# Kernel tuning notes

Hardware: AMD Instinct MI355X
Metric: run time of the kernel (lower is better)

The kernel has to match this reference:

```python
import jax, jax.numpy as jnp
import numpy as np

NUM_AGENTS = 1000
N_ACTIONS = 16
HIDDEN = 256
COMM_STEPS = 4
B, M = 1024, 64


def setup_inputs() -> dict:
    key = jax.random.key(0)
    ks = jax.random.split(key, 8)
    agent_ids = jax.random.randint(ks[0], (B, M), 0, NUM_AGENTS)
    emb = jax.random.normal(ks[1], (NUM_AGENTS, HIDDEN), dtype=jnp.float32) * 0.1
    s1 = 1.0 / np.sqrt(3 * HIDDEN)
    W1 = jax.random.uniform(ks[2], (3 * HIDDEN, HIDDEN), jnp.float32, -s1, s1)
    b1 = jax.random.uniform(ks[3], (HIDDEN,), jnp.float32, -s1, s1)
    s2 = 1.0 / np.sqrt(HIDDEN)
    W2 = jax.random.uniform(ks[4], (HIDDEN, HIDDEN), jnp.float32, -s2, s2)
    b2 = jax.random.uniform(ks[5], (HIDDEN,), jnp.float32, -s2, s2)
    Wd = jax.random.uniform(ks[6], (HIDDEN, N_ACTIONS), jnp.float32, -s2, s2)
    bd = jax.random.uniform(ks[7], (N_ACTIONS,), jnp.float32, -s2, s2)
    return {"agent_ids": agent_ids, "emb": emb, "W1": W1, "b1": b1,
            "W2": W2, "b2": b2, "Wd": Wd, "bd": bd}


def reference(agent_ids, emb, W1, b1, W2, b2, Wd, bd):
    # h0: (B, M, H) embedding lookup
    h0 = emb[agent_ids]
    h = h0
    m = agent_ids.shape[1]
    inv = 1.0 / (m - 1)
    for _ in range(COMM_STEPS):
        # mean of other agents' hidden states: c_j = (sum_k h_k - h_j)/(M-1)
        c = (jnp.sum(h, axis=1, keepdims=True) - h) * inv
        x = jnp.concatenate([h, c, h0], axis=-1)  # (B, M, 3H)
        delta = jax.nn.relu(jnp.einsum('bmi,ih->bmh', x, W1) + b1)
        delta = jnp.einsum('bmi,ih->bmh', delta, W2) + b2
        h = h + delta  # residual (use_skip=True)
    logits = jnp.einsum('bmh,ha->bma', h, Wd) + bd
    return logits
```

## Files before the change

kernel.cpp:

```cpp
#include <hip/hip_runtime.h>

#define HID 256
#define NB 1024
#define NACT 16

typedef __bf16 bf16x8 __attribute__((ext_vector_type(8)));
typedef float  f32x4  __attribute__((ext_vector_type(4)));

#define HA_LO   32768
#define OV      65536
#define LDS_TOT 72704

#define PREP_N (4 * 65536 + 4096)

__device__ __forceinline__ unsigned short f2bf(float x) {
    union { __bf16 b; unsigned short u; } v; v.b = (__bf16)x; return v.u;
}
__device__ __forceinline__ float bf2f(unsigned short u) {
    union { unsigned short u; __bf16 b; } v; v.u = u; return (float)v.b;
}
__device__ __forceinline__ float b2f_lo(unsigned v) { return bf2f((unsigned short)(v & 0xffffu)); }
__device__ __forceinline__ float b2f_hi(unsigned v) { return bf2f((unsigned short)(v >> 16)); }
__device__ __forceinline__ unsigned pack2(float a, float b) {
    return (unsigned)f2bf(a) | ((unsigned)f2bf(b) << 16);
}

__global__ __launch_bounds__(256) void prep_k(const float* __restrict__ W1,
                                              const float* __restrict__ W2,
                                              const float* __restrict__ Wd,
                                              unsigned short* __restrict__ WAh, unsigned short* __restrict__ WAl,
                                              unsigned short* __restrict__ WHh, unsigned short* __restrict__ WHl,
                                              unsigned short* __restrict__ WBh, unsigned short* __restrict__ WBl,
                                              unsigned short* __restrict__ WDh, unsigned short* __restrict__ WDl,
                                              float* __restrict__ Wc) {
    int i = blockIdx.x * 256 + threadIdx.x;
    const float inv = 1.0f / 63.0f;
    if (i < 3 * 65536) {
        int mat = i >> 16, j = i & 65535;
        int kq = j >> 13, r = j & 8191;
        int nb = r >> 9, r2 = r & 511;
        int l = r2 >> 3, e = r2 & 7;
        int n = nb * 16 + (l & 15);
        int k = kq * 32 + (l >> 4) * 8 + e;
        float val;
        if (mat == 0)      val = W1[k * 256 + n] - inv * W1[(256 + k) * 256 + n];
        else if (mat == 1) val = W1[(512 + k) * 256 + n];
        else               val = W2[k * 256 + n];
        unsigned short hi = f2bf(val);
        unsigned short lo = f2bf(val - bf2f(hi));
        if (mat == 0)      { WAh[j] = hi; WAl[j] = lo; }
        else if (mat == 1) { WHh[j] = hi; WHl[j] = lo; }
        else               { WBh[j] = hi; WBl[j] = lo; }
    } else if (i < 4 * 65536) {
        int j = i - 3 * 65536, k = j >> 8, n = j & 255;
        Wc[j] = inv * W1[(256 + k) * 256 + n];
    } else if (i < PREP_N) {
        int j = i - 4 * 65536, a = j >> 8, k = j & 255;
        float val = Wd[k * 16 + a];
        unsigned short hi = f2bf(val);
        WDh[j] = hi; WDl[j] = f2bf(val - bf2f(hi));
    }
}

__device__ __forceinline__ void kloopL2(const unsigned short* __restrict__ Wfh,
                                        const unsigned short* __restrict__ Wfl,
                                        const char* hA, f32x4 (&acc)[4][2],
                                        int w, int lane, int l15, int g)
{
    const int rxA = (l15 & 7) << 4;
    const size_t lbase = ((size_t)(w * 2) * 64 + lane) * 8;
    #pragma unroll 2
    for (int kq = 0; kq < 8; ++kq) {
        const int cb = (kq * 64 + g * 16) ^ rxA;
        bf16x8 ah[4], al[4];
        #pragma unroll
        for (int mt = 0; mt < 4; ++mt) {
            int rb = (mt * 16 + l15) * 512;
            ah[mt] = *(const bf16x8*)(hA + rb + cb);
            al[mt] = *(const bf16x8*)(hA + HA_LO + rb + cb);
        }
        const size_t kb = (size_t)kq * 8192 + lbase;
        #pragma unroll
        for (int nt = 0; nt < 2; ++nt) {
            bf16x8 bh = *(const bf16x8*)(Wfh + kb + nt * 512);
            bf16x8 bl = *(const bf16x8*)(Wfl + kb + nt * 512);
            #pragma unroll
            for (int mt = 0; mt < 4; ++mt) {
                acc[mt][nt] = __builtin_amdgcn_mfma_f32_16x16x32_bf16(bh, ah[mt], acc[mt][nt], 0, 0, 0);
                acc[mt][nt] = __builtin_amdgcn_mfma_f32_16x16x32_bf16(bh, al[mt], acc[mt][nt], 0, 0, 0);
                acc[mt][nt] = __builtin_amdgcn_mfma_f32_16x16x32_bf16(bl, ah[mt], acc[mt][nt], 0, 0, 0);
            }
        }
    }
}

__device__ __forceinline__ void STfun(char* lds, const float* __restrict__ Wc, int tid)
{
    char* hA = lds;
    float* Sp = (float*)(lds + OV);
    float* Sf = (float*)(lds + OV + 4096);
    float* Tp = (float*)(lds + OV + 5120);
    __syncthreads();
    {
        int ww = tid & 127, gq = tid >> 7;
        float s0 = 0.f, s1 = 0.f;
        #pragma unroll 4
        for (int m = gq * 16; m < gq * 16 + 16; ++m) {
            int byte = m * 512 + ((ww * 4) ^ ((m & 7) << 4));
            unsigned vh = *(const unsigned*)(hA + byte);
            unsigned vl = *(const unsigned*)(hA + HA_LO + byte);
            s0 += b2f_lo(vh) + b2f_lo(vl);
            s1 += b2f_hi(vh) + b2f_hi(vl);
        }
        Sp[gq * 256 + ww * 2] = s0;
        Sp[gq * 256 + ww * 2 + 1] = s1;
    }
    __syncthreads();
    if (tid < 256) Sf[tid] = (Sp[tid] + Sp[256 + tid]) + (Sp[512 + tid] + Sp[768 + tid]);
    __syncthreads();
    {
        int n = tid & 255, kh = tid >> 8;
        float a = 0.f;
        #pragma unroll 8
        for (int k = kh * 128; k < kh * 128 + 128; ++k)
            a += Sf[k] * Wc[(k << 8) + n];
        Tp[kh * 256 + n] = a;
    }
    __syncthreads();
}

__global__ __launch_bounds__(512, 2) void fused_all(
    const int* __restrict__ ids, const float* __restrict__ emb,
    const unsigned short* __restrict__ WAh, const unsigned short* __restrict__ WAl,
    const unsigned short* __restrict__ WHh, const unsigned short* __restrict__ WHl,
    const unsigned short* __restrict__ WBh, const unsigned short* __restrict__ WBl,
    const unsigned short* __restrict__ WDh, const unsigned short* __restrict__ WDl,
    const float* __restrict__ Wc,
    const float* __restrict__ b1, const float* __restrict__ b2,
    const float* __restrict__ bd, float* __restrict__ out)
{
    __shared__ __align__(16) char lds[LDS_TOT];
    const int tid = threadIdx.x;
    const int lane = tid & 63;
    const int w = tid >> 6;
    const int l15 = lane & 15, g = lane >> 4;
    const size_t rowbase = (size_t)blockIdx.x * 64;
    char* hA = lds;
    float* Tp = (float*)(lds + OV + 5120);

    {
        int r = tid >> 3, c0 = (tid & 7) * 32;
        int rx = (r & 7) << 4;
        const float4* src = (const float4*)(emb + (size_t)ids[rowbase + r] * HID + c0);
        char* dh = hA + r * 512;
        #pragma unroll
        for (int j = 0; j < 8; ++j) {
            float4 v = src[j];
            unsigned short h0 = f2bf(v.x), h1 = f2bf(v.y), h2 = f2bf(v.z), h3 = f2bf(v.w);
            unsigned short q0 = f2bf(v.x - bf2f(h0)), q1 = f2bf(v.y - bf2f(h1)),
                           q2 = f2bf(v.z - bf2f(h2)), q3 = f2bf(v.w - bf2f(h3));
            int byte = ((c0 + j * 4) * 2) ^ rx;
            *(uint2*)(dh + byte) = make_uint2((unsigned)h0 | ((unsigned)h1 << 16),
                                             (unsigned)h2 | ((unsigned)h3 << 16));
            *(uint2*)(dh + HA_LO + byte) = make_uint2((unsigned)q0 | ((unsigned)q1 << 16),
                                                      (unsigned)q2 | ((unsigned)q3 << 16));
        }
    }

    const int cb0 = w * 32 + g * 4;

    STfun(lds, Wc, tid);
    f32x4 tvr[2];
    #pragma unroll
    for (int nt = 0; nt < 2; ++nt) {
        int col = cb0 + nt * 16;
        tvr[nt] = *(const f32x4*)(Tp + col) + *(const f32x4*)(Tp + 256 + col);
    }

    f32x4 acc[4][2], u0r[4][2];
    #pragma unroll
    for (int mt = 0; mt < 4; ++mt)
        #pragma unroll
        for (int nt = 0; nt < 2; ++nt) acc[mt][nt] = (f32x4){0.f, 0.f, 0.f, 0.f};

    for (int s = 0; s < 4; ++s) {
        if (s == 0) {
            kloopL2(WHh, WHl, hA, acc, w, lane, l15, g);
            #pragma unroll
            for (int nt = 0; nt < 2; ++nt) {
                f32x4 b1v = *(const f32x4*)(b1 + cb0 + nt * 16);
                #pragma unroll
                for (int mt = 0; mt < 4; ++mt) {
                    u0r[mt][nt] = acc[mt][nt] + b1v;
                    acc[mt][nt] = (f32x4){0.f, 0.f, 0.f, 0.f};
                }
            }
        }
        #pragma unroll
        for (int mt = 0; mt < 4; ++mt)
            #pragma unroll
            for (int nt = 0; nt < 2; ++nt)
                acc[mt][nt] = tvr[nt] + u0r[mt][nt];
        kloopL2(WAh, WAl, hA, acc, w, lane, l15, g);

        __syncthreads();
        {
            f32x4 b2v0 = *(const f32x4*)(b2 + cb0);
            f32x4 b2v1 = *(const f32x4*)(b2 + cb0 + 16);
            #pragma unroll
            for (int mt = 0; mt < 4; ++mt)
                #pragma unroll
                for (int nt = 0; nt < 2; ++nt) {
                    int row = mt * 16 + l15;
                    int byte = row * 512 + (((cb0 + nt * 16) * 2) ^ ((l15 & 7) << 4));
                    uint2 ph = *(const uint2*)(hA + byte);
                    uint2 pl = *(const uint2*)(hA + HA_LO + byte);
                    f32x4 hres;
                    hres[0] = b2f_lo(ph.x) + b2f_lo(pl.x);
                    hres[1] = b2f_hi(ph.x) + b2f_hi(pl.x);
                    hres[2] = b2f_lo(ph.y) + b2f_lo(pl.y);
                    hres[3] = b2f_hi(ph.y) + b2f_hi(pl.y);
                    f32x4 av = acc[mt][nt];
                    float a0 = fmaxf(av[0], 0.f), a1 = fmaxf(av[1], 0.f);
                    float a2 = fmaxf(av[2], 0.f), a3 = fmaxf(av[3], 0.f);
                    unsigned h01 = pack2(a0, a1), h23 = pack2(a2, a3);
                    float r0 = a0 - bf2f((unsigned short)h01);
                    float r1 = a1 - bf2f((unsigned short)(h01 >> 16));
                    float r2 = a2 - bf2f((unsigned short)h23);
                    float r3 = a3 - bf2f((unsigned short)(h23 >> 16));
                    *(uint2*)(hA + byte) = make_uint2(h01, h23);
                    *(uint2*)(hA + HA_LO + byte) = make_uint2(pack2(r0, r1), pack2(r2, r3));
                    acc[mt][nt] = hres + (nt ? b2v1 : b2v0);
                }
        }
        __syncthreads();

        kloopL2(WBh, WBl, hA, acc, w, lane, l15, g);

        __syncthreads();
        #pragma unroll
        for (int mt = 0; mt < 4; ++mt)
            #pragma unroll
            for (int nt = 0; nt < 2; ++nt) {
                int row = mt * 16 + l15;
                int byte = row * 512 + (((cb0 + nt * 16) * 2) ^ ((l15 & 7) << 4));
                f32x4 av = acc[mt][nt];
                unsigned h01 = pack2(av[0], av[1]), h23 = pack2(av[2], av[3]);
                float r0 = av[0] - bf2f((unsigned short)h01);
                float r1 = av[1] - bf2f((unsigned short)(h01 >> 16));
                float r2 = av[2] - bf2f((unsigned short)h23);
                float r3 = av[3] - bf2f((unsigned short)(h23 >> 16));
                *(uint2*)(hA + byte) = make_uint2(h01, h23);
                *(uint2*)(hA + HA_LO + byte) = make_uint2(pack2(r0, r1), pack2(r2, r3));
                acc[mt][nt] = (f32x4){0.f, 0.f, 0.f, 0.f};
            }

        if (s < 3) {
            STfun(lds, Wc, tid);
            #pragma unroll
            for (int nt = 0; nt < 2; ++nt) {
                int col = cb0 + nt * 16;
                tvr[nt] = *(const f32x4*)(Tp + col) + *(const f32x4*)(Tp + 256 + col);
            }
        }
    }

    __syncthreads();
    if (w < 4) {
        const int rx = (l15 & 7) << 4;
        f32x4 dacc = (f32x4){0.f, 0.f, 0.f, 0.f};
        #pragma unroll 2
        for (int kq = 0; kq < 8; ++kq) {
            int byte = (w * 16 + l15) * 512 + ((kq * 64 + g * 16) ^ rx);
            bf16x8 hh = *(const bf16x8*)(hA + byte);
            bf16x8 hl = *(const bf16x8*)(hA + HA_LO + byte);
            const int k = kq * 32;
            bf16x8 wdh = *(const bf16x8*)(WDh + (size_t)l15 * 256 + k + g * 8);
            bf16x8 wdl = *(const bf16x8*)(WDl + (size_t)l15 * 256 + k + g * 8);
            dacc = __builtin_amdgcn_mfma_f32_16x16x32_bf16(wdh, hh, dacc, 0, 0, 0);
            dacc = __builtin_amdgcn_mfma_f32_16x16x32_bf16(wdh, hl, dacc, 0, 0, 0);
            dacc = __builtin_amdgcn_mfma_f32_16x16x32_bf16(wdl, hh, dacc, 0, 0, 0);
        }
        f32x4 bdv = *(const f32x4*)(bd + g * 4);
        f32x4 o = dacc + bdv;
        *(f32x4*)(out + (rowbase + w * 16 + l15) * NACT + g * 4) = o;
    }
}

extern "C" void kernel_launch(void* const* d_in, const int* in_sizes, int n_in,
                              void* d_out, int out_size, void* d_ws, size_t ws_size,
                              hipStream_t stream) {
    const int*   ids = (const int*)d_in[0];
    const float* emb = (const float*)d_in[1];
    const float* W1  = (const float*)d_in[2];
    const float* b1  = (const float*)d_in[3];
    const float* W2  = (const float*)d_in[4];
    const float* b2  = (const float*)d_in[5];
    const float* Wd  = (const float*)d_in[6];
    const float* bd  = (const float*)d_in[7];
    float* out = (float*)d_out;

    char* p = (char*)d_ws;
    unsigned short* WAh = (unsigned short*)p; p += 65536 * 2;
    unsigned short* WAl = (unsigned short*)p; p += 65536 * 2;
    unsigned short* WHh = (unsigned short*)p; p += 65536 * 2;
    unsigned short* WHl = (unsigned short*)p; p += 65536 * 2;
    unsigned short* WBh = (unsigned short*)p; p += 65536 * 2;
    unsigned short* WBl = (unsigned short*)p; p += 65536 * 2;
    unsigned short* WDh = (unsigned short*)p; p += 4096 * 2;
    unsigned short* WDl = (unsigned short*)p; p += 4096 * 2;
    float* Wc = (float*)p;

    prep_k<<<(PREP_N + 255) / 256, 256, 0, stream>>>(W1, W2, Wd, WAh, WAl, WHh, WHl,
                                                     WBh, WBl, WDh, WDl, Wc);
    fused_all<<<NB, 512, 0, stream>>>(ids, emb, WAh, WAl, WHh, WHl, WBh, WBl,
                                      WDh, WDl, Wc, b1, b2, bd, out);
}
```

Measured before the change: 278.1 us.

## Compute column-sum correction via MFMA and shuffle reductions, pad LDS rows

Replaces the scalar FP32 Sf·Wc matvec, which ran with several block barriers each step, with split-bf16 MFMA on a newly prepped WCh/WCl weight pair. The next step's column sums now come from the register accumulators through xor-shuffle reductions instead of a separate LDS pass. The XOR-swizzled LDS layout becomes a padded row stride of 528 bytes, and total LDS use drops. The cost is extra MFMA work per step with a broadcast B operand, plus the risk that the new padded stride causes different bank conflicts.

```diff
diff --git a/kernel.cpp b/kernel.cpp
--- a/kernel.cpp
+++ b/kernel.cpp
@@ -3,13 +3,14 @@
 #define HID 256
 #define NB 1024
 #define NACT 16
+#define HSTRIDE 528
 
 typedef __bf16 bf16x8 __attribute__((ext_vector_type(8)));
 typedef float  f32x4  __attribute__((ext_vector_type(4)));
 
-#define HA_LO   32768
-#define OV      65536
-#define LDS_TOT 72704
+#define HA_LO   33792
+#define S_OFF   67584
+#define LDS_TOT 68608
 
 #define PREP_N (4 * 65536 + 4096)
 
@@ -31,11 +32,11 @@
                                               unsigned short* __restrict__ WAh, unsigned short* __restrict__ WAl,
                                               unsigned short* __restrict__ WHh, unsigned short* __restrict__ WHl,
                                               unsigned short* __restrict__ WBh, unsigned short* __restrict__ WBl,
-                                              unsigned short* __restrict__ WDh, unsigned short* __restrict__ WDl,
-                                              float* __restrict__ Wc) {
+                                              unsigned short* __restrict__ WCh, unsigned short* __restrict__ WCl,
+                                              unsigned short* __restrict__ WDh, unsigned short* __restrict__ WDl) {
     int i = blockIdx.x * 256 + threadIdx.x;
     const float inv = 1.0f / 63.0f;
-    if (i < 3 * 65536) {
+    if (i < 4 * 65536) {
         int mat = i >> 16, j = i & 65535;
         int kq = j >> 13, r = j & 8191;
         int nb = r >> 9, r2 = r & 511;
@@ -45,15 +46,14 @@
         float val;
         if (mat == 0)      val = W1[k * 256 + n] - inv * W1[(256 + k) * 256 + n];
         else if (mat == 1) val = W1[(512 + k) * 256 + n];
-        else               val = W2[k * 256 + n];
+        else if (mat == 2) val = W2[k * 256 + n];
+        else               val = inv * W1[(256 + k) * 256 + n];
         unsigned short hi = f2bf(val);
         unsigned short lo = f2bf(val - bf2f(hi));
         if (mat == 0)      { WAh[j] = hi; WAl[j] = lo; }
         else if (mat == 1) { WHh[j] = hi; WHl[j] = lo; }
-        else               { WBh[j] = hi; WBl[j] = lo; }
-    } else if (i < 4 * 65536) {
-        int j = i - 3 * 65536, k = j >> 8, n = j & 255;
-        Wc[j] = inv * W1[(256 + k) * 256 + n];
+        else if (mat == 2) { WBh[j] = hi; WBl[j] = lo; }
+        else               { WCh[j] = hi; WCl[j] = lo; }
     } else if (i < PREP_N) {
         int j = i - 4 * 65536, a = j >> 8, k = j & 255;
         float val = Wd[k * 16 + a];
@@ -65,17 +65,15 @@
 __device__ __forceinline__ void kloopL2(const unsigned short* __restrict__ Wfh,
                                         const unsigned short* __restrict__ Wfl,
                                         const char* hA, f32x4 (&acc)[4][2],
-                                        int w, int lane, int l15, int g)
+                                        size_t lbase, int l15, int g)
 {
-    const int rxA = (l15 & 7) << 4;
-    const size_t lbase = ((size_t)(w * 2) * 64 + lane) * 8;
     #pragma unroll 2
     for (int kq = 0; kq < 8; ++kq) {
-        const int cb = (kq * 64 + g * 16) ^ rxA;
+        const int cb = kq * 64 + g * 16;
         bf16x8 ah[4], al[4];
         #pragma unroll
         for (int mt = 0; mt < 4; ++mt) {
-            int rb = (mt * 16 + l15) * 512;
+            int rb = (mt * 16 + l15) * HSTRIDE;
             ah[mt] = *(const bf16x8*)(hA + rb + cb);
             al[mt] = *(const bf16x8*)(hA + HA_LO + rb + cb);
         }
@@ -92,41 +90,6 @@
             }
         }
     }
-}
-
-__device__ __forceinline__ void STfun(char* lds, const float* __restrict__ Wc, int tid)
-{
-    char* hA = lds;
-    float* Sp = (float*)(lds + OV);
-    float* Sf = (float*)(lds + OV + 4096);
-    float* Tp = (float*)(lds + OV + 5120);
-    __syncthreads();
-    {
-        int ww = tid & 127, gq = tid >> 7;
-        float s0 = 0.f, s1 = 0.f;
-        #pragma unroll 4
-        for (int m = gq * 16; m < gq * 16 + 16; ++m) {
-            int byte = m * 512 + ((ww * 4) ^ ((m & 7) << 4));
-            unsigned vh = *(const unsigned*)(hA + byte);
-            unsigned vl = *(const unsigned*)(hA + HA_LO + byte);
-            s0 += b2f_lo(vh) + b2f_lo(vl);
-            s1 += b2f_hi(vh) + b2f_hi(vl);
-        }
-        Sp[gq * 256 + ww * 2] = s0;
-        Sp[gq * 256 + ww * 2 + 1] = s1;
-    }
-    __syncthreads();
-    if (tid < 256) Sf[tid] = (Sp[tid] + Sp[256 + tid]) + (Sp[512 + tid] + Sp[768 + tid]);
-    __syncthreads();
-    {
-        int n = tid & 255, kh = tid >> 8;
-        float a = 0.f;
-        #pragma unroll 8
-        for (int k = kh * 128; k < kh * 128 + 128; ++k)
-            a += Sf[k] * Wc[(k << 8) + n];
-        Tp[kh * 256 + n] = a;
-    }
-    __syncthreads();
 }
 
 __global__ __launch_bounds__(512, 2) void fused_all(
@@ -134,8 +97,8 @@
     const unsigned short* __restrict__ WAh, const unsigned short* __restrict__ WAl,
     const unsigned short* __restrict__ WHh, const unsigned short* __restrict__ WHl,
     const unsigned short* __restrict__ WBh, const unsigned short* __restrict__ WBl,
+    const unsigned short* __restrict__ WCh, const unsigned short* __restrict__ WCl,
     const unsigned short* __restrict__ WDh, const unsigned short* __restrict__ WDl,
-    const float* __restrict__ Wc,
     const float* __restrict__ b1, const float* __restrict__ b2,
     const float* __restrict__ bd, float* __restrict__ out)
 {
@@ -146,36 +109,39 @@
     const int l15 = lane & 15, g = lane >> 4;
     const size_t rowbase = (size_t)blockIdx.x * 64;
     char* hA = lds;
-    float* Tp = (float*)(lds + OV + 5120);
+    float* Sf = (float*)(lds + S_OFF);
+    const size_t lbase = ((size_t)(w * 2) * 64 + lane) * 8;
+    const int cb0 = w * 32 + g * 4;
 
     {
         int r = tid >> 3, c0 = (tid & 7) * 32;
-        int rx = (r & 7) << 4;
         const float4* src = (const float4*)(emb + (size_t)ids[rowbase + r] * HID + c0);
-        char* dh = hA + r * 512;
+        char* dh = hA + r * HSTRIDE + c0 * 2;
         #pragma unroll
         for (int j = 0; j < 8; ++j) {
             float4 v = src[j];
             unsigned short h0 = f2bf(v.x), h1 = f2bf(v.y), h2 = f2bf(v.z), h3 = f2bf(v.w);
             unsigned short q0 = f2bf(v.x - bf2f(h0)), q1 = f2bf(v.y - bf2f(h1)),
                            q2 = f2bf(v.z - bf2f(h2)), q3 = f2bf(v.w - bf2f(h3));
-            int byte = ((c0 + j * 4) * 2) ^ rx;
-            *(uint2*)(dh + byte) = make_uint2((unsigned)h0 | ((unsigned)h1 << 16),
-                                             (unsigned)h2 | ((unsigned)h3 << 16));
-            *(uint2*)(dh + HA_LO + byte) = make_uint2((unsigned)q0 | ((unsigned)q1 << 16),
-                                                      (unsigned)q2 | ((unsigned)q3 << 16));
-        }
-    }
-
-    const int cb0 = w * 32 + g * 4;
-
-    STfun(lds, Wc, tid);
-    f32x4 tvr[2];
-    #pragma unroll
-    for (int nt = 0; nt < 2; ++nt) {
-        int col = cb0 + nt * 16;
-        tvr[nt] = *(const f32x4*)(Tp + col) + *(const f32x4*)(Tp + 256 + col);
-    }
+            *(uint2*)(dh + j * 8) = make_uint2((unsigned)h0 | ((unsigned)h1 << 16),
+                                               (unsigned)h2 | ((unsigned)h3 << 16));
+            *(uint2*)(dh + HA_LO + j * 8) = make_uint2((unsigned)q0 | ((unsigned)q1 << 16),
+                                                       (unsigned)q2 | ((unsigned)q3 << 16));
+        }
+    }
+    __syncthreads();
+
+    if (tid < 256) {
+        float ssum = 0.f;
+        #pragma unroll 8
+        for (int m = 0; m < 64; ++m) {
+            int byte = m * HSTRIDE + tid * 2;
+            ssum += bf2f(*(const unsigned short*)(hA + byte))
+                  + bf2f(*(const unsigned short*)(hA + HA_LO + byte));
+        }
+        Sf[tid] = ssum;
+    }
+    __syncthreads();
 
     f32x4 acc[4][2], u0r[4][2];
     #pragma unroll
@@ -183,25 +149,48 @@
         #pragma unroll
         for (int nt = 0; nt < 2; ++nt) acc[mt][nt] = (f32x4){0.f, 0.f, 0.f, 0.f};
 
+    kloopL2(WHh, WHl, hA, acc, lbase, l15, g);
+    #pragma unroll
+    for (int nt = 0; nt < 2; ++nt) {
+        f32x4 b1v = *(const f32x4*)(b1 + cb0 + nt * 16);
+        #pragma unroll
+        for (int mt = 0; mt < 4; ++mt)
+            u0r[mt][nt] = acc[mt][nt] + b1v;
+    }
+
     for (int s = 0; s < 4; ++s) {
-        if (s == 0) {
-            kloopL2(WHh, WHl, hA, acc, w, lane, l15, g);
+        f32x4 tacc[2];
+        tacc[0] = tacc[1] = (f32x4){0.f, 0.f, 0.f, 0.f};
+        #pragma unroll 2
+        for (int kq = 0; kq < 8; ++kq) {
+            const float* sp = Sf + kq * 32 + g * 8;
+            f32x4 sa = *(const f32x4*)sp;
+            f32x4 sb = *(const f32x4*)(sp + 4);
+            bf16x8 shv, slv;
+            #pragma unroll
+            for (int e = 0; e < 8; ++e) {
+                float sv = (e < 4) ? sa[e] : sb[e - 4];
+                unsigned short h = f2bf(sv);
+                ((unsigned short*)&shv)[e] = h;
+                ((unsigned short*)&slv)[e] = f2bf(sv - bf2f(h));
+            }
+            const size_t kb = (size_t)kq * 8192 + lbase;
             #pragma unroll
             for (int nt = 0; nt < 2; ++nt) {
-                f32x4 b1v = *(const f32x4*)(b1 + cb0 + nt * 16);
-                #pragma unroll
-                for (int mt = 0; mt < 4; ++mt) {
-                    u0r[mt][nt] = acc[mt][nt] + b1v;
-                    acc[mt][nt] = (f32x4){0.f, 0.f, 0.f, 0.f};
-                }
-            }
-        }
+                bf16x8 wch = *(const bf16x8*)(WCh + kb + nt * 512);
+                bf16x8 wcl = *(const bf16x8*)(WCl + kb + nt * 512);
+                tacc[nt] = __builtin_amdgcn_mfma_f32_16x16x32_bf16(wch, shv, tacc[nt], 0, 0, 0);
+                tacc[nt] = __builtin_amdgcn_mfma_f32_16x16x32_bf16(wch, slv, tacc[nt], 0, 0, 0);
+                tacc[nt] = __builtin_amdgcn_mfma_f32_16x16x32_bf16(wcl, shv, tacc[nt], 0, 0, 0);
+            }
+        }
+
         #pragma unroll
         for (int mt = 0; mt < 4; ++mt)
             #pragma unroll
             for (int nt = 0; nt < 2; ++nt)
-                acc[mt][nt] = tvr[nt] + u0r[mt][nt];
-        kloopL2(WAh, WAl, hA, acc, w, lane, l15, g);
+                acc[mt][nt] = u0r[mt][nt] + tacc[nt];
+        kloopL2(WAh, WAl, hA, acc, lbase, l15, g);
 
         __syncthreads();
         {
@@ -211,8 +200,7 @@
             for (int mt = 0; mt < 4; ++mt)
                 #pragma unroll
                 for (int nt = 0; nt < 2; ++nt) {
-                    int row = mt * 16 + l15;
-                    int byte = row * 512 + (((cb0 + nt * 16) * 2) ^ ((l15 & 7) << 4));
+                    int byte = (mt * 16 + l15) * HSTRIDE + (cb0 + nt * 16) * 2;
                     uint2 ph = *(const uint2*)(hA + byte);
                     uint2 pl = *(const uint2*)(hA + HA_LO + byte);
                     f32x4 hres;
@@ -235,15 +223,14 @@
         }
         __syncthreads();
 
-        kloopL2(WBh, WBl, hA, acc, w, lane, l15, g);
+        kloopL2(WBh, WBl, hA, acc, lbase, l15, g);
 
         __syncthreads();
         #pragma unroll
         for (int mt = 0; mt < 4; ++mt)
             #pragma unroll
             for (int nt = 0; nt < 2; ++nt) {
-                int row = mt * 16 + l15;
-                int byte = row * 512 + (((cb0 + nt * 16) * 2) ^ ((l15 & 7) << 4));
+                int byte = (mt * 16 + l15) * HSTRIDE + (cb0 + nt * 16) * 2;
                 f32x4 av = acc[mt][nt];
                 unsigned h01 = pack2(av[0], av[1]), h23 = pack2(av[2], av[3]);
                 float r0 = av[0] - bf2f((unsigned short)h01);
@@ -252,26 +239,29 @@
                 float r3 = av[3] - bf2f((unsigned short)(h23 >> 16));
                 *(uint2*)(hA + byte) = make_uint2(h01, h23);
                 *(uint2*)(hA + HA_LO + byte) = make_uint2(pack2(r0, r1), pack2(r2, r3));
-                acc[mt][nt] = (f32x4){0.f, 0.f, 0.f, 0.f};
-            }
-
+            }
         if (s < 3) {
-            STfun(lds, Wc, tid);
             #pragma unroll
             for (int nt = 0; nt < 2; ++nt) {
-                int col = cb0 + nt * 16;
-                tvr[nt] = *(const f32x4*)(Tp + col) + *(const f32x4*)(Tp + 256 + col);
-            }
-        }
-    }
-
-    __syncthreads();
+                f32x4 cs = (acc[0][nt] + acc[1][nt]) + (acc[2][nt] + acc[3][nt]);
+                #pragma unroll
+                for (int d = 1; d < 16; d <<= 1) {
+                    cs[0] += __shfl_xor(cs[0], d);
+                    cs[1] += __shfl_xor(cs[1], d);
+                    cs[2] += __shfl_xor(cs[2], d);
+                    cs[3] += __shfl_xor(cs[3], d);
+                }
+                if (l15 == 0) *(f32x4*)(Sf + cb0 + nt * 16) = cs;
+            }
+        }
+        __syncthreads();
+    }
+
     if (w < 4) {
-        const int rx = (l15 & 7) << 4;
         f32x4 dacc = (f32x4){0.f, 0.f, 0.f, 0.f};
         #pragma unroll 2
         for (int kq = 0; kq < 8; ++kq) {
-            int byte = (w * 16 + l15) * 512 + ((kq * 64 + g * 16) ^ rx);
+            int byte = (w * 16 + l15) * HSTRIDE + kq * 64 + g * 16;
             bf16x8 hh = *(const bf16x8*)(hA + byte);
             bf16x8 hl = *(const bf16x8*)(hA + HA_LO + byte);
             const int k = kq * 32;
@@ -307,12 +297,13 @@
     unsigned short* WHl = (unsigned short*)p; p += 65536 * 2;
     unsigned short* WBh = (unsigned short*)p; p += 65536 * 2;
     unsigned short* WBl = (unsigned short*)p; p += 65536 * 2;
+    unsigned short* WCh = (unsigned short*)p; p += 65536 * 2;
+    unsigned short* WCl = (unsigned short*)p; p += 65536 * 2;
     unsigned short* WDh = (unsigned short*)p; p += 4096 * 2;
     unsigned short* WDl = (unsigned short*)p; p += 4096 * 2;
-    float* Wc = (float*)p;
 
     prep_k<<<(PREP_N + 255) / 256, 256, 0, stream>>>(W1, W2, Wd, WAh, WAl, WHh, WHl,
-                                                     WBh, WBl, WDh, WDl, Wc);
+                                                     WBh, WBl, WCh, WCl, WDh, WDl);
     fused_all<<<NB, 512, 0, stream>>>(ids, emb, WAh, WAl, WHh, WHl, WBh, WBl,
-                                      WDh, WDl, Wc, b1, b2, bd, out);
-}
+                                      WCh, WCl, WDh, WDl, b1, b2, bd, out);
+}
```

Result: faster. 266.2 us (-4.3%).
